# Kernel optimization log

Measured on AMD Instinct MI355X. Metric: run time of the kernel, lower is better.

The kernel has to match this reference:

```python
import jax, jax.numpy as jnp
import numpy as np

N_FULL, N_LOCAL, N_GLOBAL = 6, 4, 2
N_HEADS = N_FULL + N_LOCAL + N_GLOBAL
WINDOW = 64
DIM = 1536
B, S = 2, 2048


def setup_inputs() -> dict:
    key = jax.random.key(0)
    k0, k1, k2 = jax.random.split(key, 3)
    sc = DIM ** -0.5
    return {
        "x": jax.random.normal(k0, (B, S, DIM), dtype=jnp.float32),
        "Wqkv": jax.random.normal(k1, (DIM, 3 * DIM), dtype=jnp.float32) * sc,
        "bqkv": jnp.zeros((3 * DIM,), dtype=jnp.float32),
        "Wout": jax.random.normal(k2, (DIM, DIM), dtype=jnp.float32) * sc,
        "bout": jnp.zeros((DIM,), dtype=jnp.float32),
    }


def _attend(q, k, v, scale, bias=None):
    # q,k,v: [B,H,S,D]
    scores = jnp.einsum("bhqd,bhkd->bhqk", q, k) * scale
    if bias is not None:
        scores = scores + bias
    p = jax.nn.softmax(scores, axis=-1)
    return jnp.einsum("bhqk,bhkd->bhqd", p, v)


def reference(x, Wqkv, bqkv, Wout, bout):
    Bb, Ss, D = x.shape
    hd = D // N_HEADS
    scale = hd ** -0.5
    qkv = (x @ Wqkv + bqkv).reshape(Bb, Ss, 3, N_HEADS, hd)
    qkv = jnp.transpose(qkv, (2, 0, 3, 1, 4))  # [3,B,H,S,hd]
    q, k, v = qkv[0], qkv[1], qkv[2]
    h1 = N_FULL
    h2 = N_FULL + N_LOCAL

    # tier 1: full attention on first n_full heads
    out_full = _attend(q[:, :h1], k[:, :h1], v[:, :h1], scale)

    # tier 2: sliding-window (|i-j| <= window//2 allowed) on next n_local heads
    idx = jnp.arange(Ss)
    allowed = jnp.abs(idx[:, None] - idx[None, :]) <= WINDOW // 2  # [S,S]
    bias = jnp.where(allowed, 0.0, -jnp.inf).astype(x.dtype)[None, None]
    out_local = _attend(q[:, h1:h2], k[:, h1:h2], v[:, h1:h2], scale, bias)

    # tier 3: global — attend only to first and last tokens
    kg = jnp.stack([k[:, h2:, 0], k[:, h2:, -1]], axis=2)  # [B,Hg,2,hd]
    vg = jnp.stack([v[:, h2:, 0], v[:, h2:, -1]], axis=2)
    out_global = _attend(q[:, h2:], kg, vg, scale)

    out = jnp.concatenate([out_full, out_local, out_global], axis=1)  # [B,H,S,hd]
    out = jnp.transpose(out, (0, 2, 1, 3)).reshape(Bb, Ss, D)
    return out @ Wout + bout
```

## Files before the change

kernel.cpp:

```cpp
#include <hip/hip_runtime.h>
#include <hip/hip_bf16.h>

#define SEQ    2048
#define TOK    4096
#define DMODEL 1536
#define QKVROW 4608
#define HD     128
#define SCALE  0.08838834764831845f

#define NSPLIT 4
#define KRANGE (SEQ / NSPLIT)
#define NPAIR  12
#define ROWS_P (NPAIR * SEQ)
#define OPART_ELEMS ((size_t)ROWS_P * HD)

typedef __attribute__((ext_vector_type(8))) short short8;
typedef __attribute__((ext_vector_type(4))) short short4v;
typedef __attribute__((ext_vector_type(4))) float f32x4;

__device__ __forceinline__ float b2f(short s) {
    union { unsigned u; float f; } x;
    x.u = ((unsigned)(unsigned short)s) << 16;
    return x.f;
}
__device__ __forceinline__ short f2b(float f) {
    union { float f; unsigned u; } x; x.f = f;
    unsigned u = x.u;
    unsigned r = (u + 0x7fffu + ((u >> 16) & 1u)) >> 16;
    return (short)r;
}

__device__ __forceinline__ void gld_lds16(const short* g, short* l) {
    __builtin_amdgcn_global_load_lds(
        (__attribute__((address_space(1))) void*)(g),
        (__attribute__((address_space(3))) void*)(l), 16, 0, 0);
}

#define CVT_BLOCKS  6144
#define TQKV_BLOCKS 1728
#define TOUT_BLOCKS 576

__device__ __forceinline__ void transpose_tile(
    const float* __restrict__ W, short* __restrict__ WT,
    int K, int N, int k0, int n0, int t, short (*tile)[65])
{
    {
        int j  = t & 63;
        int i0 = (t >> 6) * 16;
        for (int ii = 0; ii < 16; ++ii)
            tile[i0 + ii][j] = f2b(W[(size_t)(k0 + i0 + ii) * N + n0 + j]);
    }
    __syncthreads();
    {
        int i  = t & 63;
        int j0 = (t >> 6) * 16;
        for (int jj = 0; jj < 16; ++jj)
            WT[(size_t)(n0 + j0 + jj) * K + k0 + i] = tile[i][j0 + jj];
    }
}

__global__ __launch_bounds__(256) void prepass_k(
    const float* __restrict__ x, const float* __restrict__ Wqkv,
    const float* __restrict__ Wout, short* __restrict__ xb,
    short* __restrict__ WqkvT, short* __restrict__ WoutT)
{
    __shared__ short tile[64][65];
    const int bid = blockIdx.x;
    const int t   = threadIdx.x;
    if (bid < CVT_BLOCKS) {
        int i = bid * 1024 + t * 4;
        float4 v = *(const float4*)(x + i);
        short4v b = { f2b(v.x), f2b(v.y), f2b(v.z), f2b(v.w) };
        *(short4v*)(xb + i) = b;
    } else if (bid < CVT_BLOCKS + TQKV_BLOCKS) {
        int tb = bid - CVT_BLOCKS;
        transpose_tile(Wqkv, WqkvT, DMODEL, QKVROW,
                       (tb / (QKVROW / 64)) * 64, (tb % (QKVROW / 64)) * 64, t, tile);
    } else {
        int tb = bid - (CVT_BLOCKS + TQKV_BLOCKS);
        transpose_tile(Wout, WoutT, DMODEL, DMODEL,
                       (tb / (DMODEL / 64)) * 64, (tb % (DMODEL / 64)) * 64, t, tile);
    }
}

#define LD_A(S, G)                                                            \
    do {                                                                      \
        af[0] = *(const short8*)(smem + ((S) * 8 + wm * 4 + (G) * 2) * 512 + lane * 8); \
        af[1] = *(const short8*)(smem + ((S) * 8 + wm * 4 + (G) * 2 + 1) * 512 + lane * 8); \
    } while (0)
#define LD_B(S)                                                               \
    do {                                                                      \
        for (int ni = 0; ni < 4; ++ni)                                        \
            bf[ni] = *(const short8*)(smem + 8192 + ((S) * 16 + wn4 + ni) * 512 + lane * 8); \
    } while (0)
#define MFMA_G(G)                                                             \
    do {                                                                      \
        __builtin_amdgcn_s_setprio(1);                                        \
        for (int mi = 0; mi < 2; ++mi)                                        \
            for (int ni = 0; ni < 4; ++ni)                                    \
                acc[(G) * 2 + mi][ni] = __builtin_amdgcn_mfma_f32_16x16x32_bf16( \
                    af[mi], bf[ni], acc[(G) * 2 + mi][ni], 0, 0, 0);          \
        __builtin_amdgcn_s_setprio(0);                                        \
    } while (0)
#define STG(S, KT)                                                            \
    do {                                                                      \
        gld_lds16(gA0 + (KT) * 32, smem + ((S) * 8 + wave) * 512);            \
        gld_lds16(gB0 + (KT) * 32, smem + 8192 + ((S) * 16 + wave) * 512);    \
        gld_lds16(gB1 + (KT) * 32, smem + 8192 + ((S) * 16 + 8 + wave) * 512);\
    } while (0)
#define BAR                                                                   \
    do {                                                                      \
        asm volatile("" ::: "memory");                                        \
        __builtin_amdgcn_s_barrier();                                         \
        asm volatile("" ::: "memory");                                        \
    } while (0)
#define VM0 asm volatile("s_waitcnt vmcnt(0)" ::: "memory")

template <bool OUT_BF16, int MT, int NT>
__global__ __launch_bounds__(512, 4) void gemm_2ph(
    const short* __restrict__ A, const short* __restrict__ BT,
    const float* __restrict__ bias, void* __restrict__ Cout,
    int N, int K)
{
    __shared__ short smem[24576];

    constexpr int NWG = MT * NT;
    constexpr int Q8  = NWG / 8, R8 = NWG % 8;
    constexpr int BW  = 4;
    constexpr int FULLB = NT / BW;
    constexpr int TB  = FULLB * MT * BW;
    constexpr int TW  = NT - FULLB * BW;
    const int orig = blockIdx.x;
    const int xcd  = orig & 7, idx = orig >> 3;
    const int wg   = (xcd < R8 ? xcd * (Q8 + 1) : R8 * (Q8 + 1) + (xcd - R8) * Q8) + idx;
    int mt, nt;
    if (TW == 0 || wg < TB) {
        int band = wg / (MT * BW);
        int rem  = wg % (MT * BW);
        mt = rem / BW;
        nt = band * BW + rem % BW;
    } else {
        constexpr int TWD = TW ? TW : 1;
        int rem = wg - TB;
        mt = rem / TWD;
        nt = FULLB * BW + rem % TWD;
    }
    const int bm0 = mt * 128;
    const int bn0 = nt * 256;

    const int t    = threadIdx.x;
    const int wave = t >> 6;
    const int lane = t & 63;
    const int quad = lane >> 4;
    const int lo   = lane & 15;
    const int wm   = wave >> 2;
    const int wn   = wave & 3;
    const int wn4  = wn * 4;

    const int rO = quad * 8;
    const short* gA0 = A  + (size_t)(bm0 + wave * 16 + lo) * K + rO;
    const short* gB0 = BT + (size_t)(bn0 + wave * 16 + lo) * K + rO;
    const short* gB1 = BT + (size_t)(bn0 + (8 + wave) * 16 + lo) * K + rO;

    f32x4 acc[4][4];
#pragma unroll
    for (int i = 0; i < 4; ++i)
#pragma unroll
        for (int j = 0; j < 4; ++j)
            acc[i][j] = (f32x4){0.f, 0.f, 0.f, 0.f};

    const int NTK = K >> 5;

    STG(0, 0);
    VM0;
    BAR;

    short8 af[2], bf[4];
#pragma unroll 1
    for (int it = 0; it < (NTK >> 1); ++it) {
        const int t1 = 2 * it + 1;
        const int t2 = min(2 * it + 2, NTK - 1);
        LD_B(0); LD_A(0, 0);
        STG(1, t1);
        MFMA_G(0);
        BAR;
        LD_A(0, 1);
        MFMA_G(1);
        VM0;
        BAR;
        LD_B(1); LD_A(1, 0);
        STG(0, t2);
        MFMA_G(0);
        BAR;
        LD_A(1, 1);
        MFMA_G(1);
        VM0;
        BAR;
    }

#pragma unroll
    for (int ni = 0; ni < 4; ++ni) {
        int col  = bn0 + wn * 64 + ni * 16 + lo;
        float bv = bias[col];
#pragma unroll
        for (int a = 0; a < 4; ++a)
#pragma unroll
            for (int r = 0; r < 4; ++r) {
                int row   = bm0 + wm * 64 + a * 16 + quad * 4 + r;
                float val = acc[a][ni][r] + bv;
                if (OUT_BF16)
                    ((short*)Cout)[(size_t)row * N + col] = f2b(val);
                else
                    ((float*)Cout)[(size_t)row * N + col] = val;
            }
    }
}

#define KSP 136
#define VTP 44
#define PLP 40

__global__ __launch_bounds__(256) void attn_full_split(
    const short* __restrict__ qkv, short* __restrict__ Opart,
    float* __restrict__ lsum)
{
    const int pair = blockIdx.y;
    const int b    = pair / 6;
    const int h    = pair % 6;
    const int q0   = blockIdx.x * 64;
    const int kz   = blockIdx.z;
    const int t    = threadIdx.x;
    const int wave = t >> 6;
    const int lane = t & 63;
    const int quad = lane >> 4;
    const int lo   = lane & 15;

    __shared__ short Ks[32 * KSP];
    __shared__ short Vr[32 * KSP];
    __shared__ short Vt[128 * VTP];
    __shared__ short Pl[4][16 * PLP];

    const short* base = qkv + (size_t)b * SEQ * QKVROW;

    short8 qf[4];
    {
        int qrow = q0 + wave * 16 + lo;
        const short* qp = base + (size_t)qrow * QKVROW + h * HD;
        for (int c = 0; c < 4; ++c)
            qf[c] = *(const short8*)(qp + c * 32 + quad * 8);
    }

    f32x4 o[8];
    for (int i = 0; i < 8; ++i) o[i] = (f32x4){0.f, 0.f, 0.f, 0.f};
    float lrow[4] = {0.f, 0.f, 0.f, 0.f};

    const int skey = t >> 3;
    const int sdc  = (t & 7) * 16;
    const int thd  = t & 127;
    const int tkc  = (t >> 7) * 16;

    const int kend = kz * KRANGE + KRANGE;
    for (int k0 = kz * KRANGE; k0 < kend; k0 += 32) {
        {
            const short* kro = base + (size_t)(k0 + skey) * QKVROW + DMODEL     + h * HD + sdc;
            const short* vro = base + (size_t)(k0 + skey) * QKVROW + 2 * DMODEL + h * HD + sdc;
            short8 ka = *(const short8*)kro;
            short8 kb = *(const short8*)(kro + 8);
            short8 va = *(const short8*)vro;
            short8 vb = *(const short8*)(vro + 8);
            *(short8*)(Ks + skey * KSP + sdc)     = ka;
            *(short8*)(Ks + skey * KSP + sdc + 8) = kb;
            *(short8*)(Vr + skey * KSP + sdc)     = va;
            *(short8*)(Vr + skey * KSP + sdc + 8) = vb;
        }
        __syncthreads();

        {
            short8 x0, x1;
            for (int j = 0; j < 8; ++j) x0[j] = Vr[(tkc + j) * KSP + thd];
            for (int j = 0; j < 8; ++j) x1[j] = Vr[(tkc + 8 + j) * KSP + thd];
            *(short8*)(Vt + thd * VTP + tkc)     = x0;
            *(short8*)(Vt + thd * VTP + tkc + 8) = x1;
        }

        f32x4 s[2];
        s[0] = (f32x4){0.f, 0.f, 0.f, 0.f};
        s[1] = (f32x4){0.f, 0.f, 0.f, 0.f};
        for (int g = 0; g < 2; ++g)
            for (int c = 0; c < 4; ++c) {
                short8 kf = *(const short8*)(Ks + (g * 16 + lo) * KSP + c * 32 + quad * 8);
                s[g] = __builtin_amdgcn_mfma_f32_16x16x32_bf16(qf[c], kf, s[g], 0, 0, 0);
            }

        for (int g = 0; g < 2; ++g)
            for (int r = 0; r < 4; ++r) {
                float p = __expf(s[g][r] * SCALE);
                lrow[r] += p;
                Pl[wave][(quad * 4 + r) * PLP + g * 16 + lo] = f2b(p);
            }
        __syncthreads();

        short8 pf = *(const short8*)(&Pl[wave][lo * PLP + quad * 8]);
        for (int ni = 0; ni < 8; ++ni) {
            short8 vf = *(const short8*)(Vt + (ni * 16 + lo) * VTP + quad * 8);
            o[ni] = __builtin_amdgcn_mfma_f32_16x16x32_bf16(pf, vf, o[ni], 0, 0, 0);
        }
    }

    for (int r = 0; r < 4; ++r)
        for (int off = 1; off < 16; off <<= 1)
            lrow[r] += __shfl_xor(lrow[r], off, 64);

    for (int ni = 0; ni < 8; ++ni)
        for (int r = 0; r < 4; ++r) {
            int grow = pair * SEQ + q0 + wave * 16 + quad * 4 + r;
            Opart[(size_t)kz * OPART_ELEMS + (size_t)grow * HD + ni * 16 + lo] =
                f2b(o[ni][r]);
        }
    if (lo == 0)
        for (int r = 0; r < 4; ++r) {
            int grow = pair * SEQ + q0 + wave * 16 + quad * 4 + r;
            lsum[kz * ROWS_P + grow] = lrow[r];
        }
}

__global__ __launch_bounds__(256) void attn_local_mfma(
    const short* __restrict__ qkv, short* __restrict__ att)
{
    const int pair = blockIdx.y;
    const int b    = pair >> 2;
    const int h    = 6 + (pair & 3);
    const int q0   = blockIdx.x * 64;
    const int t    = threadIdx.x;
    const int wave = t >> 6;
    const int lane = t & 63;
    const int quad = lane >> 4;
    const int lo   = lane & 15;

    __shared__ short Ks[32 * KSP];
    __shared__ short Vr[32 * KSP];
    __shared__ short Vt[128 * VTP];
    __shared__ short Pl[4][16 * PLP];

    const short* base = qkv + (size_t)b * SEQ * QKVROW;

    short8 qf[4];
    {
        int qrow = q0 + wave * 16 + lo;
        const short* qp = base + (size_t)qrow * QKVROW + h * HD;
        for (int c = 0; c < 4; ++c)
            qf[c] = *(const short8*)(qp + c * 32 + quad * 8);
    }

    f32x4 o[8];
    for (int i = 0; i < 8; ++i) o[i] = (f32x4){0.f, 0.f, 0.f, 0.f};
    float lrow[4] = {0.f, 0.f, 0.f, 0.f};

    const int skey = t >> 3;
    const int sdc  = (t & 7) * 16;
    const int thd  = t & 127;
    const int tkc  = (t >> 7) * 16;
    const int irow = q0 + wave * 16 + quad * 4;

    const int ks = max(0, q0 - 32);
    const int ke = min(SEQ, q0 + 96);
    for (int k0 = ks; k0 < ke; k0 += 32) {
        {
            const short* kro = base + (size_t)(k0 + skey) * QKVROW + DMODEL     + h * HD + sdc;
            const short* vro = base + (size_t)(k0 + skey) * QKVROW + 2 * DMODEL + h * HD + sdc;
            short8 ka = *(const short8*)kro;
            short8 kb = *(const short8*)(kro + 8);
            short8 va = *(const short8*)vro;
            short8 vb = *(const short8*)(vro + 8);
            *(short8*)(Ks + skey * KSP + sdc)     = ka;
            *(short8*)(Ks + skey * KSP + sdc + 8) = kb;
            *(short8*)(Vr + skey * KSP + sdc)     = va;
            *(short8*)(Vr + skey * KSP + sdc + 8) = vb;
        }
        __syncthreads();

        {
            short8 x0, x1;
            for (int j = 0; j < 8; ++j) x0[j] = Vr[(tkc + j) * KSP + thd];
            for (int j = 0; j < 8; ++j) x1[j] = Vr[(tkc + 8 + j) * KSP + thd];
            *(short8*)(Vt + thd * VTP + tkc)     = x0;
            *(short8*)(Vt + thd * VTP + tkc + 8) = x1;
        }

        f32x4 s[2];
        s[0] = (f32x4){0.f, 0.f, 0.f, 0.f};
        s[1] = (f32x4){0.f, 0.f, 0.f, 0.f};
        for (int g = 0; g < 2; ++g)
            for (int c = 0; c < 4; ++c) {
                short8 kf = *(const short8*)(Ks + (g * 16 + lo) * KSP + c * 32 + quad * 8);
                s[g] = __builtin_amdgcn_mfma_f32_16x16x32_bf16(qf[c], kf, s[g], 0, 0, 0);
            }

        for (int g = 0; g < 2; ++g)
            for (int r = 0; r < 4; ++r) {
                int j = k0 + g * 16 + lo;
                int d = irow + r - j;
                float p = (d >= -32 && d <= 32) ? __expf(s[g][r] * SCALE) : 0.f;
                lrow[r] += p;
                Pl[wave][(quad * 4 + r) * PLP + g * 16 + lo] = f2b(p);
            }
        __syncthreads();

        short8 pf = *(const short8*)(&Pl[wave][lo * PLP + quad * 8]);
        for (int ni = 0; ni < 8; ++ni) {
            short8 vf = *(const short8*)(Vt + (ni * 16 + lo) * VTP + quad * 8);
            o[ni] = __builtin_amdgcn_mfma_f32_16x16x32_bf16(pf, vf, o[ni], 0, 0, 0);
        }
    }

    for (int r = 0; r < 4; ++r)
        for (int off = 1; off < 16; off <<= 1)
            lrow[r] += __shfl_xor(lrow[r], off, 64);

    for (int ni = 0; ni < 8; ++ni)
        for (int r = 0; r < 4; ++r) {
            int row = irow + r;
            size_t off = ((size_t)(b * SEQ + row)) * DMODEL + h * HD + ni * 16 + lo;
            att[off] = f2b(o[ni][r] / lrow[r]);
        }
}

#define MERGE_BLOCKS  12288
#define GLOBAL_BLOCKS 2048

__global__ __launch_bounds__(256) void postattn_k(
    const short* __restrict__ qkv, const short* __restrict__ Opart,
    const float* __restrict__ lsum, short* __restrict__ att)
{
    const int bid  = blockIdx.x;
    const int t    = threadIdx.x;
    const int wave = t >> 6;
    const int lane = t & 63;

    if (bid < MERGE_BLOCKS) {
        int idx  = bid * 256 + t;
        int pair = idx >> 18;
        int q    = (idx >> 7) & (SEQ - 1);
        int hd   = idx & (HD - 1);
        int row  = pair * SEQ + q;
        float osum = 0.f, ls = 0.f;
        for (int z = 0; z < NSPLIT; ++z) {
            ls   += lsum[z * ROWS_P + row];
            osum += b2f(Opart[(size_t)z * OPART_ELEMS + (size_t)row * HD + hd]);
        }
        int b = pair / 6, h = pair % 6;
        att[((size_t)(b * SEQ + q)) * DMODEL + h * HD + hd] = f2b(osum / ls);
    } else {
        int gb   = bid - MERGE_BLOCKS;
        int pair = gb >> 9;
        int q    = (gb & 511) * 4 + wave;
        int b    = pair >> 1;
        int h    = 10 + (pair & 1);

        const short* base = qkv + (size_t)b * SEQ * QKVROW;
        const short* qp   = base + (size_t)q * QKVROW + h * HD;
        const short* k0   = base + DMODEL + h * HD;
        const short* k1   = base + (size_t)(SEQ - 1) * QKVROW + DMODEL + h * HD;

        float s0 = fmaf(b2f(qp[lane]), b2f(k0[lane]),
                   b2f(qp[lane + 64]) * b2f(k0[lane + 64]));
        float s1 = fmaf(b2f(qp[lane]), b2f(k1[lane]),
                   b2f(qp[lane + 64]) * b2f(k1[lane + 64]));
        for (int off = 1; off < 64; off <<= 1) {
            s0 += __shfl_xor(s0, off, 64);
            s1 += __shfl_xor(s1, off, 64);
        }
        s0 *= SCALE; s1 *= SCALE;
        float m  = fmaxf(s0, s1);
        float e0 = __expf(s0 - m), e1 = __expf(s1 - m);
        float inv = 1.f / (e0 + e1);
        float p0 = e0 * inv, p1 = e1 * inv;

        const short* v0 = base + 2 * DMODEL + h * HD;
        const short* v1 = base + (size_t)(SEQ - 1) * QKVROW + 2 * DMODEL + h * HD;
        size_t ob = ((size_t)(b * SEQ + q)) * DMODEL + h * HD;
        att[ob + lane]      = f2b(fmaf(p0, b2f(v0[lane]),      p1 * b2f(v1[lane])));
        att[ob + lane + 64] = f2b(fmaf(p0, b2f(v0[lane + 64]), p1 * b2f(v1[lane + 64])));
    }
}

extern "C" void kernel_launch(void* const* d_in, const int* in_sizes, int n_in,
                              void* d_out, int out_size, void* d_ws, size_t ws_size,
                              hipStream_t stream) {
    const float* x    = (const float*)d_in[0];
    const float* Wqkv = (const float*)d_in[1];
    const float* bqkv = (const float*)d_in[2];
    const float* Wout = (const float*)d_in[3];
    const float* bout = (const float*)d_in[4];

    char* p = (char*)d_ws;
    short* qkv   = (short*)p;  p += (size_t)TOK * QKVROW * 2;
    short* Opart = (short*)p;  p += OPART_ELEMS * NSPLIT * 2;
    float* lsum  = (float*)p;  p += (size_t)ROWS_P * NSPLIT * 4;
    short* xb    = (short*)p;  p += (size_t)TOK * DMODEL * 2;
    short* att   = xb;
    short* WqkvT = (short*)p;  p += (size_t)QKVROW * DMODEL * 2;
    short* WoutT = (short*)p;

    prepass_k<<<dim3(CVT_BLOCKS + TQKV_BLOCKS + TOUT_BLOCKS), 256, 0, stream>>>(
        x, Wqkv, Wout, xb, WqkvT, WoutT);
    gemm_2ph<true, 32, 18><<<dim3(32 * 18), 512, 0, stream>>>(
        xb, WqkvT, bqkv, (void*)qkv, QKVROW, DMODEL);
    attn_full_split<<<dim3(SEQ / 64, NPAIR, NSPLIT), 256, 0, stream>>>(qkv, Opart, lsum);
    attn_local_mfma<<<dim3(SEQ / 64, 8), 256, 0, stream>>>(qkv, att);
    postattn_k<<<dim3(MERGE_BLOCKS + GLOBAL_BLOCKS), 256, 0, stream>>>(
        qkv, Opart, lsum, att);
    gemm_2ph<false, 32, 6><<<dim3(32 * 6), 512, 0, stream>>>(
        att, WoutT, bout, d_out, DMODEL, DMODEL);
}
```

Baseline: 353.1 us.

## Replace 128x256 two-phase GEMM with 64x256 double-buffered 4-wave GEMM

Both projection GEMMs now use 64-row by 256-column tiles computed by 256-thread workgroups instead of 128x256 tiles on 512 threads. The main loop becomes a simple per-k-tile double buffer with a single __syncthreads, dropping the split two-phase schedule, explicit vmcnt waits and s_setprio hints. The grid doubles, which is meant to improve load balance and occupancy across CUs. In exchange each B tile is reused by fewer output rows, so there is more global and LDS traffic per flop.

```diff
diff --git a/kernel.cpp b/kernel.cpp
--- a/kernel.cpp
+++ b/kernel.cpp
@@ -83,46 +83,13 @@
     }
 }
 
-#define LD_A(S, G)                                                            \
-    do {                                                                      \
-        af[0] = *(const short8*)(smem + ((S) * 8 + wm * 4 + (G) * 2) * 512 + lane * 8); \
-        af[1] = *(const short8*)(smem + ((S) * 8 + wm * 4 + (G) * 2 + 1) * 512 + lane * 8); \
-    } while (0)
-#define LD_B(S)                                                               \
-    do {                                                                      \
-        for (int ni = 0; ni < 4; ++ni)                                        \
-            bf[ni] = *(const short8*)(smem + 8192 + ((S) * 16 + wn4 + ni) * 512 + lane * 8); \
-    } while (0)
-#define MFMA_G(G)                                                             \
-    do {                                                                      \
-        __builtin_amdgcn_s_setprio(1);                                        \
-        for (int mi = 0; mi < 2; ++mi)                                        \
-            for (int ni = 0; ni < 4; ++ni)                                    \
-                acc[(G) * 2 + mi][ni] = __builtin_amdgcn_mfma_f32_16x16x32_bf16( \
-                    af[mi], bf[ni], acc[(G) * 2 + mi][ni], 0, 0, 0);          \
-        __builtin_amdgcn_s_setprio(0);                                        \
-    } while (0)
-#define STG(S, KT)                                                            \
-    do {                                                                      \
-        gld_lds16(gA0 + (KT) * 32, smem + ((S) * 8 + wave) * 512);            \
-        gld_lds16(gB0 + (KT) * 32, smem + 8192 + ((S) * 16 + wave) * 512);    \
-        gld_lds16(gB1 + (KT) * 32, smem + 8192 + ((S) * 16 + 8 + wave) * 512);\
-    } while (0)
-#define BAR                                                                   \
-    do {                                                                      \
-        asm volatile("" ::: "memory");                                        \
-        __builtin_amdgcn_s_barrier();                                         \
-        asm volatile("" ::: "memory");                                        \
-    } while (0)
-#define VM0 asm volatile("s_waitcnt vmcnt(0)" ::: "memory")
-
 template <bool OUT_BF16, int MT, int NT>
-__global__ __launch_bounds__(512, 4) void gemm_2ph(
+__global__ __launch_bounds__(256, 4) void gemm_db(
     const short* __restrict__ A, const short* __restrict__ BT,
     const float* __restrict__ bias, void* __restrict__ Cout,
     int N, int K)
 {
-    __shared__ short smem[24576];
+    __shared__ short smem[20480];
 
     constexpr int NWG = MT * NT;
     constexpr int Q8  = NWG / 8, R8 = NWG % 8;
@@ -145,7 +112,7 @@
         mt = rem / TWD;
         nt = FULLB * BW + rem % TWD;
     }
-    const int bm0 = mt * 128;
+    const int bm0 = mt * 64;
     const int bn0 = nt * 256;
 
     const int t    = threadIdx.x;
@@ -153,14 +120,14 @@
     const int lane = t & 63;
     const int quad = lane >> 4;
     const int lo   = lane & 15;
-    const int wm   = wave >> 2;
-    const int wn   = wave & 3;
-    const int wn4  = wn * 4;
+
+    auto ldsA = [&](int s, int st) { return smem + (s * 4 + st) * 512; };
+    auto ldsB = [&](int s, int st) { return smem + 4096 + (s * 16 + st) * 512; };
 
     const int rO = quad * 8;
     const short* gA0 = A  + (size_t)(bm0 + wave * 16 + lo) * K + rO;
-    const short* gB0 = BT + (size_t)(bn0 + wave * 16 + lo) * K + rO;
-    const short* gB1 = BT + (size_t)(bn0 + (8 + wave) * 16 + lo) * K + rO;
+    const short* gB0 = BT + (size_t)(bn0 + wave * 64 + lo) * K + rO;
+    const int bstep = 16 * K;
 
     f32x4 acc[4][4];
 #pragma unroll
@@ -171,42 +138,54 @@
 
     const int NTK = K >> 5;
 
+#define STG(S, KT)                                                         \
+    do {                                                                   \
+        gld_lds16(gA0 + (KT) * 32, ldsA((S), wave));                       \
+        for (int j = 0; j < 4; ++j)                                        \
+            gld_lds16(gB0 + j * bstep + (KT) * 32, ldsB((S), wave * 4 + j)); \
+    } while (0)
+
     STG(0, 0);
-    VM0;
-    BAR;
+    __syncthreads();
 
     short8 af[2], bf[4];
 #pragma unroll 1
-    for (int it = 0; it < (NTK >> 1); ++it) {
-        const int t1 = 2 * it + 1;
-        const int t2 = min(2 * it + 2, NTK - 1);
-        LD_B(0); LD_A(0, 0);
-        STG(1, t1);
-        MFMA_G(0);
-        BAR;
-        LD_A(0, 1);
-        MFMA_G(1);
-        VM0;
-        BAR;
-        LD_B(1); LD_A(1, 0);
-        STG(0, t2);
-        MFMA_G(0);
-        BAR;
-        LD_A(1, 1);
-        MFMA_G(1);
-        VM0;
-        BAR;
-    }
+    for (int kt = 0; kt < NTK; ++kt) {
+        const int s  = kt & 1;
+        const int nk = min(kt + 1, NTK - 1);
+#pragma unroll
+        for (int ni = 0; ni < 4; ++ni)
+            bf[ni] = *(const short8*)(ldsB(s, wave * 4 + ni) + lane * 8);
+        af[0] = *(const short8*)(ldsA(s, 0) + lane * 8);
+        af[1] = *(const short8*)(ldsA(s, 1) + lane * 8);
+        STG(s ^ 1, nk);
+#pragma unroll
+        for (int mi = 0; mi < 2; ++mi)
+#pragma unroll
+            for (int ni = 0; ni < 4; ++ni)
+                acc[mi][ni] = __builtin_amdgcn_mfma_f32_16x16x32_bf16(
+                    af[mi], bf[ni], acc[mi][ni], 0, 0, 0);
+        af[0] = *(const short8*)(ldsA(s, 2) + lane * 8);
+        af[1] = *(const short8*)(ldsA(s, 3) + lane * 8);
+#pragma unroll
+        for (int mi = 0; mi < 2; ++mi)
+#pragma unroll
+            for (int ni = 0; ni < 4; ++ni)
+                acc[2 + mi][ni] = __builtin_amdgcn_mfma_f32_16x16x32_bf16(
+                    af[mi], bf[ni], acc[2 + mi][ni], 0, 0, 0);
+        __syncthreads();
+    }
+#undef STG
 
 #pragma unroll
     for (int ni = 0; ni < 4; ++ni) {
-        int col  = bn0 + wn * 64 + ni * 16 + lo;
+        int col  = bn0 + wave * 64 + ni * 16 + lo;
         float bv = bias[col];
 #pragma unroll
         for (int a = 0; a < 4; ++a)
 #pragma unroll
             for (int r = 0; r < 4; ++r) {
-                int row   = bm0 + wm * 64 + a * 16 + quad * 4 + r;
+                int row   = bm0 + a * 16 + quad * 4 + r;
                 float val = acc[a][ni][r] + bv;
                 if (OUT_BF16)
                     ((short*)Cout)[(size_t)row * N + col] = f2b(val);
@@ -504,12 +483,12 @@
 
     prepass_k<<<dim3(CVT_BLOCKS + TQKV_BLOCKS + TOUT_BLOCKS), 256, 0, stream>>>(
         x, Wqkv, Wout, xb, WqkvT, WoutT);
-    gemm_2ph<true, 32, 18><<<dim3(32 * 18), 512, 0, stream>>>(
+    gemm_db<true, 64, 18><<<dim3(64 * 18), 256, 0, stream>>>(
         xb, WqkvT, bqkv, (void*)qkv, QKVROW, DMODEL);
     attn_full_split<<<dim3(SEQ / 64, NPAIR, NSPLIT), 256, 0, stream>>>(qkv, Opart, lsum);
     attn_local_mfma<<<dim3(SEQ / 64, 8), 256, 0, stream>>>(qkv, att);
     postattn_k<<<dim3(MERGE_BLOCKS + GLOBAL_BLOCKS), 256, 0, stream>>>(
         qkv, Opart, lsum, att);
-    gemm_2ph<false, 32, 6><<<dim3(32 * 6), 512, 0, stream>>>(
+    gemm_db<false, 64, 6><<<dim3(64 * 6), 256, 0, stream>>>(
         att, WoutT, bout, d_out, DMODEL, DMODEL);
 }
```

New measurement: 393.4 us. 11.4% more time.

## Deepen GEMM pipeline to four LDS stages with register double-buffered fragments

Applied to the files above, without the earlier changes.

Replaces the two-stage GEMM mainloop with a four-slot LDS ring, prefetching three K-tiles ahead. It waits with vmcnt(6) instead of draining all loads, and double-buffers the A/B register fragments so LDS reads for the next step overlap with the current MFMAs. The goal is to hide global-load latency. In exchange it doubles shared memory to 96KB per block and lowers the launch-bounds occupancy hint from 4 to 2, which cuts waves per CU.

```diff
diff --git a/kernel.cpp b/kernel.cpp
--- a/kernel.cpp
+++ b/kernel.cpp
@@ -83,46 +83,48 @@
     }
 }
 
-#define LD_A(S, G)                                                            \
-    do {                                                                      \
-        af[0] = *(const short8*)(smem + ((S) * 8 + wm * 4 + (G) * 2) * 512 + lane * 8); \
-        af[1] = *(const short8*)(smem + ((S) * 8 + wm * 4 + (G) * 2 + 1) * 512 + lane * 8); \
+#define STG(SL, KT)                                                        \
+    do {                                                                   \
+        gld_lds16(gA0 + (KT) * 32, smem + (SL) * 12288 + wave * 512);      \
+        gld_lds16(gB0 + (KT) * 32, smem + (SL) * 12288 + 4096 + wave * 512); \
+        gld_lds16(gB1 + (KT) * 32, smem + (SL) * 12288 + 4096 + (8 + wave) * 512); \
     } while (0)
-#define LD_B(S)                                                               \
-    do {                                                                      \
-        for (int ni = 0; ni < 4; ++ni)                                        \
-            bf[ni] = *(const short8*)(smem + 8192 + ((S) * 16 + wn4 + ni) * 512 + lane * 8); \
+#define RD_A(DST, SL, G)                                                   \
+    do {                                                                   \
+        DST[0] = *(const short8*)(smem + (SL) * 12288 + (wm4 + (G) * 2) * 512 + lane * 8); \
+        DST[1] = *(const short8*)(smem + (SL) * 12288 + (wm4 + (G) * 2 + 1) * 512 + lane * 8); \
     } while (0)
-#define MFMA_G(G)                                                             \
-    do {                                                                      \
-        __builtin_amdgcn_s_setprio(1);                                        \
-        for (int mi = 0; mi < 2; ++mi)                                        \
-            for (int ni = 0; ni < 4; ++ni)                                    \
+#define RD_B(DST, SL)                                                      \
+    do {                                                                   \
+        DST[0] = *(const short8*)(smem + (SL) * 12288 + 4096 + (wn4 + 0) * 512 + lane * 8); \
+        DST[1] = *(const short8*)(smem + (SL) * 12288 + 4096 + (wn4 + 1) * 512 + lane * 8); \
+        DST[2] = *(const short8*)(smem + (SL) * 12288 + 4096 + (wn4 + 2) * 512 + lane * 8); \
+        DST[3] = *(const short8*)(smem + (SL) * 12288 + 4096 + (wn4 + 3) * 512 + lane * 8); \
+    } while (0)
+#define MFMA_G(G, AF, BF)                                                  \
+    do {                                                                   \
+        __builtin_amdgcn_s_setprio(1);                                     \
+        for (int mi = 0; mi < 2; ++mi)                                     \
+            for (int ni = 0; ni < 4; ++ni)                                 \
                 acc[(G) * 2 + mi][ni] = __builtin_amdgcn_mfma_f32_16x16x32_bf16( \
-                    af[mi], bf[ni], acc[(G) * 2 + mi][ni], 0, 0, 0);          \
-        __builtin_amdgcn_s_setprio(0);                                        \
+                    AF[mi], BF[ni], acc[(G) * 2 + mi][ni], 0, 0, 0);       \
+        __builtin_amdgcn_s_setprio(0);                                     \
     } while (0)
-#define STG(S, KT)                                                            \
-    do {                                                                      \
-        gld_lds16(gA0 + (KT) * 32, smem + ((S) * 8 + wave) * 512);            \
-        gld_lds16(gB0 + (KT) * 32, smem + 8192 + ((S) * 16 + wave) * 512);    \
-        gld_lds16(gB1 + (KT) * 32, smem + 8192 + ((S) * 16 + 8 + wave) * 512);\
+#define BAR                                                                \
+    do {                                                                   \
+        asm volatile("" ::: "memory");                                     \
+        __builtin_amdgcn_s_barrier();                                      \
+        asm volatile("" ::: "memory");                                     \
     } while (0)
-#define BAR                                                                   \
-    do {                                                                      \
-        asm volatile("" ::: "memory");                                        \
-        __builtin_amdgcn_s_barrier();                                         \
-        asm volatile("" ::: "memory");                                        \
-    } while (0)
-#define VM0 asm volatile("s_waitcnt vmcnt(0)" ::: "memory")
+#define VMW asm volatile("s_waitcnt vmcnt(6)" ::: "memory")
 
 template <bool OUT_BF16, int MT, int NT>
-__global__ __launch_bounds__(512, 4) void gemm_2ph(
+__global__ __launch_bounds__(512, 2) void gemm_p4(
     const short* __restrict__ A, const short* __restrict__ BT,
     const float* __restrict__ bias, void* __restrict__ Cout,
     int N, int K)
 {
-    __shared__ short smem[24576];
+    __shared__ short smem[49152];
 
     constexpr int NWG = MT * NT;
     constexpr int Q8  = NWG / 8, R8 = NWG % 8;
@@ -155,6 +157,7 @@
     const int lo   = lane & 15;
     const int wm   = wave >> 2;
     const int wn   = wave & 3;
+    const int wm4  = wm * 4;
     const int wn4  = wn * 4;
 
     const int rO = quad * 8;
@@ -171,32 +174,36 @@
 
     const int NTK = K >> 5;
 
-    STG(0, 0);
-    VM0;
+    STG(0, 0); STG(1, 1); STG(2, 2);
+    VMW;
     BAR;
 
-    short8 af[2], bf[4];
+    short8 a0[2], b0[4], n0[2], a1[2], b1[4], n1[2];
+    RD_B(b0, 0); RD_A(a0, 0, 0);
+
 #pragma unroll 1
     for (int it = 0; it < (NTK >> 1); ++it) {
-        const int t1 = 2 * it + 1;
-        const int t2 = min(2 * it + 2, NTK - 1);
-        LD_B(0); LD_A(0, 0);
-        STG(1, t1);
-        MFMA_G(0);
+        const int t0  = it * 2, t1 = t0 + 1;
+        const int sl0 = t0 & 3, sl1 = t1 & 3;
+        const int s3  = (t0 + 3) & 3, s4 = (t1 + 3) & 3;
+        const int k3  = min(t0 + 3, NTK - 1), k4 = min(t1 + 3, NTK - 1);
+        const int i2  = min(t0 + 2, NTK - 1), s2 = i2 & 3;
+        RD_A(n0, sl0, 1);
+        STG(s3, k3);
+        MFMA_G(0, a0, b0);
+        VMW; BAR;
+        RD_B(b1, sl1); RD_A(a1, sl1, 0);
+        MFMA_G(1, n0, b0);
         BAR;
-        LD_A(0, 1);
-        MFMA_G(1);
-        VM0;
+        RD_A(n1, sl1, 1);
+        STG(s4, k4);
+        MFMA_G(0, a1, b1);
+        VMW; BAR;
+        RD_B(b0, s2); RD_A(a0, s2, 0);
+        MFMA_G(1, n1, b1);
         BAR;
-        LD_B(1); LD_A(1, 0);
-        STG(0, t2);
-        MFMA_G(0);
-        BAR;
-        LD_A(1, 1);
-        MFMA_G(1);
-        VM0;
-        BAR;
-    }
+    }
+    asm volatile("s_waitcnt vmcnt(0)" ::: "memory");
 
 #pragma unroll
     for (int ni = 0; ni < 4; ++ni) {
@@ -215,6 +222,12 @@
             }
     }
 }
+#undef STG
+#undef RD_A
+#undef RD_B
+#undef MFMA_G
+#undef BAR
+#undef VMW
 
 #define KSP 136
 #define VTP 44
@@ -504,12 +517,12 @@
 
     prepass_k<<<dim3(CVT_BLOCKS + TQKV_BLOCKS + TOUT_BLOCKS), 256, 0, stream>>>(
         x, Wqkv, Wout, xb, WqkvT, WoutT);
-    gemm_2ph<true, 32, 18><<<dim3(32 * 18), 512, 0, stream>>>(
+    gemm_p4<true, 32, 18><<<dim3(32 * 18), 512, 0, stream>>>(
         xb, WqkvT, bqkv, (void*)qkv, QKVROW, DMODEL);
     attn_full_split<<<dim3(SEQ / 64, NPAIR, NSPLIT), 256, 0, stream>>>(qkv, Opart, lsum);
     attn_local_mfma<<<dim3(SEQ / 64, 8), 256, 0, stream>>>(qkv, att);
     postattn_k<<<dim3(MERGE_BLOCKS + GLOBAL_BLOCKS), 256, 0, stream>>>(
         qkv, Opart, lsum, att);
-    gemm_2ph<false, 32, 6><<<dim3(32 * 6), 512, 0, stream>>>(
+    gemm_p4<false, 32, 6><<<dim3(32 * 6), 512, 0, stream>>>(
         att, WoutT, bout, d_out, DMODEL, DMODEL);
 }
```

Result: faster. 337.1 us (-4.5%).
